# Kernel optimization log

Hardware: AMD Instinct MI355X
Metric: run time of the kernel (lower is better)

## Reference

```python
import jax, jax.numpy as jnp
import numpy as np

N_NODES = 50000
N_EDGES = 1600000
H1, F1 = 6, 16   # conv1 heads/filters
H2, F2 = 6, 24   # conv2 heads/filters
D_IN = 11
NEG_SLOPE = 0.2
EPS = 1e-12


def gat_layer(x, src, dst, W, a_src, a_dst, heads, filt):
    # x: [N, Din], W: [Din, heads*filt], a_src/a_dst: [heads, filt]
    N = x.shape[0]
    h = (x @ W).reshape(N, heads, filt)                      # [N,H,F]
    alpha_s = jnp.einsum('nhf,hf->nh', h, a_src)             # [N,H]
    alpha_d = jnp.einsum('nhf,hf->nh', h, a_dst)             # [N,H]
    e = jax.nn.leaky_relu(alpha_s[src] + alpha_d[dst], NEG_SLOPE)  # [E,H]
    # softmax over incoming edges of each dst node (segment softmax)
    m = jax.ops.segment_max(e, dst, num_segments=N)          # [N,H]
    m = jnp.where(jnp.isfinite(m), m, 0.0)
    ex = jnp.exp(e - m[dst])                                 # [E,H]
    denom = jax.ops.segment_sum(ex, dst, num_segments=N)     # [N,H]
    att = ex / (denom[dst] + EPS)                            # [E,H]
    msg = h[src] * att[:, :, None]                           # [E,H,F]
    out = jax.ops.segment_sum(msg, dst, num_segments=N)      # [N,H,F]
    return jax.nn.elu(out).reshape(N, heads * filt)


def setup_inputs() -> dict:
    key = jax.random.key(0)
    ks = jax.random.split(key, 12)
    x = jax.random.normal(ks[0], (N_NODES, D_IN), dtype=jnp.float32)
    src = jax.random.randint(ks[1], (N_EDGES,), 0, N_NODES, dtype=jnp.int32)
    dst = jax.random.randint(ks[2], (N_EDGES,), 0, N_NODES, dtype=jnp.int32)
    s = 0.1
    W1 = jax.random.normal(ks[3], (D_IN, H1 * F1), dtype=jnp.float32) * s
    a1s = jax.random.normal(ks[4], (H1, F1), dtype=jnp.float32) * s
    a1d = jax.random.normal(ks[5], (H1, F1), dtype=jnp.float32) * s
    W2 = jax.random.normal(ks[6], (H1 * F1, H2 * F2), dtype=jnp.float32) * s
    a2s = jax.random.normal(ks[7], (H2, F2), dtype=jnp.float32) * s
    a2d = jax.random.normal(ks[8], (H2, F2), dtype=jnp.float32) * s
    Wd = jax.random.normal(ks[9], (H2 * F2, 1), dtype=jnp.float32) * s
    bd = jnp.zeros((1,), dtype=jnp.float32)
    return {"x": x, "src": src, "dst": dst, "W1": W1, "a1s": a1s, "a1d": a1d,
            "W2": W2, "a2s": a2s, "a2d": a2d, "Wd": Wd, "bd": bd}


def reference(x, src, dst, W1, a1s, a1d, W2, a2s, a2d, Wd, bd):
    h = gat_layer(x, src, dst, W1, a1s, a1d, H1, F1)   # [N, 96]
    h = gat_layer(h, src, dst, W2, a2s, a2d, H2, F2)   # [N, 144]
    pooled = jnp.sum(h, axis=0).reshape(1, -1)         # [1, 144]
    norm = jnp.sqrt(jnp.sum(pooled * pooled, axis=1, keepdims=True))
    pooled = pooled / jnp.maximum(norm, 1e-12)         # F.normalize
    out = pooled @ Wd + bd                             # [1, 1], linear nonlin
    return jnp.squeeze(out, axis=1)                    # [1]
```

## Files before the change

### kernel.cpp

```cpp
#include <hip/hip_runtime.h>
#include <math.h>

#define NNODES 50000
#define NEDGES 1600000
#define NB 391
#define NBP 400

__device__ __forceinline__ float lrelu(float v) { return v > 0.f ? v : 0.2f * v; }

template<int SEL>
__device__ __forceinline__ float fp8d(unsigned u) {
    return __builtin_amdgcn_cvt_f32_fp8((int)u, SEL);
}

__global__ void padx_kernel(const float* __restrict__ x, float* __restrict__ xp, int N) {
    int t = blockIdx.x * blockDim.x + threadIdx.x;
    if (t >= N * 12) return;
    int n = t / 12, k = t - n * 12;
    xp[t] = (k < 11) ? x[n * 11 + k] : 0.f;
}

template<int DIN, int H, int F>
__global__ void va_kernel(const float* __restrict__ W, const float* __restrict__ a_s,
                          const float* __restrict__ a_d, float* __restrict__ va_s,
                          float* __restrict__ va_d, int DINEFF) {
    int t = threadIdx.x;
    if (t >= DIN * 8) return;
    int k = t / 8, h = t - k * 8;
    float s = 0.f, d = 0.f;
    if (h < H && k < DINEFF) {
        for (int f = 0; f < F; ++f) {
            float w = W[k * (H * F) + h * F + f];
            s = fmaf(w, a_s[h * F + f], s);
            d = fmaf(w, a_d[h * F + f], d);
        }
    }
    va_s[t] = s;
    va_d[t] = d;
}

template<int DIN>
__global__ void alphap_kernel(const float* __restrict__ X, const float* __restrict__ va_s,
                              const float* __restrict__ va_d, float* __restrict__ asp,
                              float* __restrict__ adp, int N) {
    __shared__ float vs[DIN * 8], vd[DIN * 8];
    for (int i = threadIdx.x; i < DIN * 8; i += blockDim.x) { vs[i] = va_s[i]; vd[i] = va_d[i]; }
    __syncthreads();
    int t = blockIdx.x * blockDim.x + threadIdx.x;
    if (t >= N * 8) return;
    int n = t / 8, h = t - n * 8;
    const float* xr = X + (size_t)n * DIN;
    float s = 0.f, d = 0.f;
    for (int k = 0; k < DIN; ++k) {
        float xv = xr[k];
        s = fmaf(xv, vs[k * 8 + h], s);
        d = fmaf(xv, vd[k * 8 + h], d);
    }
    asp[t] = s;
    adp[t] = d;
}

__global__ void bucket_hist_kernel(const int* __restrict__ dst, int* __restrict__ bcnt, int E) {
    __shared__ int h[NBP];
    for (int i = threadIdx.x; i < NBP; i += blockDim.x) h[i] = 0;
    __syncthreads();
    for (int e = blockIdx.x * blockDim.x + threadIdx.x; e < E; e += gridDim.x * blockDim.x)
        atomicAdd(&h[dst[e] >> 7], 1);
    __syncthreads();
    for (int i = threadIdx.x; i < NB; i += blockDim.x)
        if (h[i]) atomicAdd(&bcnt[i], h[i]);
}

__global__ void bucket_scan_kernel(const int* __restrict__ bcnt, int* __restrict__ bbase,
                                   int* __restrict__ bcur, int* __restrict__ off, int E) {
    __shared__ int ls[512];
    int t = threadIdx.x;
    int c = (t < NB) ? bcnt[t] : 0;
    ls[t] = c;
    __syncthreads();
    for (int o = 1; o < 512; o <<= 1) {
        int u = (t >= o) ? ls[t - o] : 0;
        __syncthreads();
        ls[t] += u;
        __syncthreads();
    }
    if (t < NB) {
        int ex = ls[t] - c;
        bbase[t] = ex;
        bcur[t] = ex;
    }
    if (t == 0) { bbase[NB] = E; off[NNODES] = E; }
}

#define BA_CHUNK 8192
#define BA_THREADS 1024
__global__ void binA_kernel(const int* __restrict__ src, const int* __restrict__ dst,
                            int* __restrict__ bcur, unsigned* __restrict__ tmp, int E) {
    __shared__ unsigned sv[BA_CHUNK];
    __shared__ unsigned short sb[BA_CHUNK];
    __shared__ int cnt[NBP], basel[NBP];
    int tid = threadIdx.x;
    for (int i = tid; i < NBP; i += BA_THREADS) cnt[i] = 0;
    __syncthreads();
    int e0 = blockIdx.x * BA_CHUNK;
    int lim = min(BA_CHUNK, E - e0);
#pragma unroll
    for (int k = 0; k < BA_CHUNK / BA_THREADS; ++k) {
        int i = k * BA_THREADS + tid;
        if (i < lim) {
            int s = src[e0 + i], d = dst[e0 + i];
            sv[i] = (unsigned)s | ((unsigned)(d & 127) << 17);
            int b = d >> 7;
            sb[i] = (unsigned short)b;
            atomicAdd(&cnt[b], 1);
        }
    }
    __syncthreads();
    for (int i = tid; i < NB; i += BA_THREADS)
        basel[i] = cnt[i] ? atomicAdd(&bcur[i], cnt[i]) : 0;
    __syncthreads();
#pragma unroll
    for (int k = 0; k < BA_CHUNK / BA_THREADS; ++k) {
        int i = k * BA_THREADS + tid;
        if (i < lim) {
            int pos = atomicAdd(&basel[sb[i]], 1);
            tmp[pos] = sv[i];
        }
    }
}

__global__ void binB_kernel(const int* __restrict__ bbase, const unsigned* __restrict__ tmp,
                            int* __restrict__ off, int* __restrict__ esrc, int N) {
    __shared__ int ncnt[128], ncur[128], ls[128];
    int b = blockIdx.x;
    int tid = threadIdx.x;
    int lo = bbase[b], hi = bbase[b + 1];
    if (tid < 128) ncnt[tid] = 0;
    __syncthreads();
    for (int i = lo + tid; i < hi; i += 256)
        atomicAdd(&ncnt[tmp[i] >> 17], 1);
    __syncthreads();
    if (tid < 128) ls[tid] = ncnt[tid];
    __syncthreads();
    for (int o = 1; o < 128; o <<= 1) {
        int u = (tid >= o && tid < 128) ? ls[tid - o] : 0;
        __syncthreads();
        if (tid < 128) ls[tid] += u;
        __syncthreads();
    }
    if (tid < 128) {
        int ex = lo + ls[tid] - ncnt[tid];
        int n = b * 128 + tid;
        if (n < N) off[n] = ex;
        ncur[tid] = ex;
    }
    __syncthreads();
    for (int i = lo + tid; i < hi; i += 256) {
        unsigned v = tmp[i];
        int pos = atomicAdd(&ncur[v >> 17], 1);
        esrc[pos] = (int)(v & 0x1FFFFu);
    }
}

#define G1_NODES 128
#define G1_THREADS (G1_NODES * 3)
#define G1_ECAP 4800
__global__ void gather1_kernel(const int* __restrict__ off, const int* __restrict__ esrc,
                               const float* __restrict__ asp, const float* __restrict__ adp,
                               const float* __restrict__ xp, float* __restrict__ aggX, int N) {
    __shared__ int se[G1_ECAP];
    int li = threadIdx.x;
    int n0 = blockIdx.x * G1_NODES;
    int nend = min(n0 + G1_NODES, N);
    int base = off[n0];
    int cnt = off[nend] - base;
    bool staged = (cnt <= G1_ECAP);
    if (staged) for (int i = li; i < cnt; i += G1_THREADS) se[i] = esrc[base + i];
    __syncthreads();
    int node = n0 + li / 3;
    int j = li % 3;
    if (node >= N) return;
    const float4 advA = *(const float4*)(adp + (size_t)node * 8);
    const float2 advB = *(const float2*)(adp + (size_t)node * 8 + 4);
    const float4* xp4 = (const float4*)xp;
    int p0 = off[node], p1 = off[node + 1];
    float4 ac[6];
    float d[6];
#pragma unroll
    for (int u = 0; u < 6; ++u) { ac[u] = make_float4(0.f, 0.f, 0.f, 0.f); d[u] = 0.f; }
#define G1_EDGE(asA, asB, xv)                                                        \
    {                                                                                \
        float a0 = __expf(lrelu(asA.x + advA.x));                                    \
        float a1 = __expf(lrelu(asA.y + advA.y));                                    \
        float a2 = __expf(lrelu(asA.z + advA.z));                                    \
        float a3 = __expf(lrelu(asA.w + advA.w));                                    \
        float a4 = __expf(lrelu(asB.x + advB.x));                                    \
        float a5 = __expf(lrelu(asB.y + advB.y));                                    \
        d[0] += a0; d[1] += a1; d[2] += a2; d[3] += a3; d[4] += a4; d[5] += a5;      \
        ac[0].x = fmaf(a0, xv.x, ac[0].x); ac[0].y = fmaf(a0, xv.y, ac[0].y);        \
        ac[0].z = fmaf(a0, xv.z, ac[0].z); ac[0].w = fmaf(a0, xv.w, ac[0].w);        \
        ac[1].x = fmaf(a1, xv.x, ac[1].x); ac[1].y = fmaf(a1, xv.y, ac[1].y);        \
        ac[1].z = fmaf(a1, xv.z, ac[1].z); ac[1].w = fmaf(a1, xv.w, ac[1].w);        \
        ac[2].x = fmaf(a2, xv.x, ac[2].x); ac[2].y = fmaf(a2, xv.y, ac[2].y);        \
        ac[2].z = fmaf(a2, xv.z, ac[2].z); ac[2].w = fmaf(a2, xv.w, ac[2].w);        \
        ac[3].x = fmaf(a3, xv.x, ac[3].x); ac[3].y = fmaf(a3, xv.y, ac[3].y);        \
        ac[3].z = fmaf(a3, xv.z, ac[3].z); ac[3].w = fmaf(a3, xv.w, ac[3].w);        \
        ac[4].x = fmaf(a4, xv.x, ac[4].x); ac[4].y = fmaf(a4, xv.y, ac[4].y);        \
        ac[4].z = fmaf(a4, xv.z, ac[4].z); ac[4].w = fmaf(a4, xv.w, ac[4].w);        \
        ac[5].x = fmaf(a5, xv.x, ac[5].x); ac[5].y = fmaf(a5, xv.y, ac[5].y);        \
        ac[5].z = fmaf(a5, xv.z, ac[5].z); ac[5].w = fmaf(a5, xv.w, ac[5].w);        \
    }
#define G1_LOOP(FS)                                                                  \
    {                                                                                \
        for (; q + 4 <= qe; q += 4) {                                                \
            int s0 = FS(q), s1 = FS(q + 1), s2 = FS(q + 2), s3 = FS(q + 3);          \
            float4 A0 = *(const float4*)(asp + (size_t)s0 * 8);                      \
            float2 B0 = *(const float2*)(asp + (size_t)s0 * 8 + 4);                  \
            float4 X0 = xp4[(size_t)s0 * 3 + j];                                     \
            float4 A1 = *(const float4*)(asp + (size_t)s1 * 8);                      \
            float2 B1 = *(const float2*)(asp + (size_t)s1 * 8 + 4);                  \
            float4 X1 = xp4[(size_t)s1 * 3 + j];                                     \
            float4 A2 = *(const float4*)(asp + (size_t)s2 * 8);                      \
            float2 B2 = *(const float2*)(asp + (size_t)s2 * 8 + 4);                  \
            float4 X2 = xp4[(size_t)s2 * 3 + j];                                     \
            float4 A3 = *(const float4*)(asp + (size_t)s3 * 8);                      \
            float2 B3 = *(const float2*)(asp + (size_t)s3 * 8 + 4);                  \
            float4 X3 = xp4[(size_t)s3 * 3 + j];                                     \
            G1_EDGE(A0, B0, X0) G1_EDGE(A1, B1, X1)                                  \
            G1_EDGE(A2, B2, X2) G1_EDGE(A3, B3, X3)                                  \
        }                                                                            \
        for (; q < qe; ++q) {                                                        \
            int s0 = FS(q);                                                          \
            float4 A0 = *(const float4*)(asp + (size_t)s0 * 8);                      \
            float2 B0 = *(const float2*)(asp + (size_t)s0 * 8 + 4);                  \
            float4 X0 = xp4[(size_t)s0 * 3 + j];                                     \
            G1_EDGE(A0, B0, X0)                                                      \
        }                                                                            \
    }
#define G1_SE(i) se[i]
#define G1_GE(i) esrc[i]
    if (staged) {
        int q = p0 - base, qe = p1 - base;
        G1_LOOP(G1_SE)
    } else {
        int q = p0, qe = p1;
        G1_LOOP(G1_GE)
    }
#undef G1_EDGE
#undef G1_LOOP
    float4* o4 = (float4*)aggX;
#pragma unroll
    for (int u = 0; u < 6; ++u) {
        float r = 1.f / (d[u] + 1e-12f);
        float4 a = ac[u];
        a.x *= r; a.y *= r; a.z *= r; a.w *= r;
        o4[((size_t)node * 6 + u) * 3 + j] = a;
    }
}

__global__ void gemmL1_kernel(const float* __restrict__ aggX, const float* __restrict__ W1,
                              float* __restrict__ out1, int N) {
    __shared__ float Wl[12 * 96];
    for (int i = threadIdx.x; i < 12 * 96; i += blockDim.x) Wl[i] = (i < 11 * 96) ? W1[i] : 0.f;
    __syncthreads();
    int t = blockIdx.x * blockDim.x + threadIdx.x;
    if (t >= N * 24) return;
    int n = t / 24, q = t - n * 24;
    int h = q / 4, c = q * 4;
    const float* ag = aggX + ((size_t)n * 6 + h) * 12;
    float4 acc = {0, 0, 0, 0};
#pragma unroll
    for (int k = 0; k < 12; ++k) {
        float xv = ag[k];
        acc.x = fmaf(xv, Wl[k * 96 + c + 0], acc.x);
        acc.y = fmaf(xv, Wl[k * 96 + c + 1], acc.y);
        acc.z = fmaf(xv, Wl[k * 96 + c + 2], acc.z);
        acc.w = fmaf(xv, Wl[k * 96 + c + 3], acc.w);
    }
    acc.x = acc.x > 0.f ? acc.x : expm1f(acc.x);
    acc.y = acc.y > 0.f ? acc.y : expm1f(acc.y);
    acc.z = acc.z > 0.f ? acc.z : expm1f(acc.z);
    acc.w = acc.w > 0.f ? acc.w : expm1f(acc.w);
    ((float4*)out1)[(size_t)n * 24 + q] = acc;
}

template<int DIN, int C, int NPT>
__global__ void gemm_fp8_kernel(const float* __restrict__ X, const float* __restrict__ W,
                                unsigned* __restrict__ Out, int N) {
    constexpr int Q = C / 4;
    __shared__ float4 Wl[DIN * Q];
    for (int i = threadIdx.x; i < DIN * Q; i += blockDim.x) Wl[i] = ((const float4*)W)[i];
    __syncthreads();
    int t = blockIdx.x * blockDim.x + threadIdx.x;
    int g = t / Q, q = t - g * Q;
    int n0 = g * NPT;
    if (n0 >= N) return;
    const float4* X4 = (const float4*)X;
    float4 acc[NPT];
#pragma unroll
    for (int u = 0; u < NPT; ++u) acc[u] = make_float4(0.f, 0.f, 0.f, 0.f);
#pragma unroll 2
    for (int k4 = 0; k4 < DIN / 4; ++k4) {
        float4 xv[NPT];
#pragma unroll
        for (int u = 0; u < NPT; ++u) xv[u] = X4[(size_t)(n0 + u) * (DIN / 4) + k4];
#pragma unroll
        for (int i = 0; i < 4; ++i) {
            float4 w = Wl[(k4 * 4 + i) * Q + q];
#pragma unroll
            for (int u = 0; u < NPT; ++u) {
                float xs = (i == 0) ? xv[u].x : (i == 1) ? xv[u].y : (i == 2) ? xv[u].z : xv[u].w;
                acc[u].x = fmaf(xs, w.x, acc[u].x);
                acc[u].y = fmaf(xs, w.y, acc[u].y);
                acc[u].z = fmaf(xs, w.z, acc[u].z);
                acc[u].w = fmaf(xs, w.w, acc[u].w);
            }
        }
    }
#pragma unroll
    for (int u = 0; u < NPT; ++u) {
        int pk = __builtin_amdgcn_cvt_pk_fp8_f32(acc[u].x, acc[u].y, 0, false);
        pk     = __builtin_amdgcn_cvt_pk_fp8_f32(acc[u].z, acc[u].w, pk, true);
        Out[(size_t)(n0 + u) * Q + q] = (unsigned)pk;
    }
}

#define G2_NODES 32
#define G2_TPN 18
#define G2_THREADS (G2_NODES * G2_TPN)
#define G2_ECAP 1600
__global__ void gather2_kernel(const int* __restrict__ off, const int* __restrict__ esrc,
                               const float* __restrict__ asp, const float* __restrict__ adp,
                               const uint2* __restrict__ h2t2, float* __restrict__ pooled, int N) {
    __shared__ float sp[144];
    __shared__ int se[G2_ECAP];
    int li = threadIdx.x;
    int n0 = blockIdx.x * G2_NODES;
    int nend = min(n0 + G2_NODES, N);
    int base = off[n0];
    int cnt = off[nend] - base;
    bool staged = (cnt <= G2_ECAP);
    if (staged) for (int i = li; i < cnt; i += G2_THREADS) se[i] = esrc[base + i];
    if (li < 144) sp[li] = 0.f;
    __syncthreads();
    int node = n0 + li / G2_TPN;
    int j = li % G2_TPN;
    if (node < N) {
        int h = j / 3;
        float adv = adp[(size_t)node * 8 + h];
        int p0 = off[node], p1 = off[node + 1];
        float acc[8];
#pragma unroll
        for (int c = 0; c < 8; ++c) acc[c] = 0.f;
        float den = 0.f;
#define G2_EDGE(ev, v)                                                     \
    {                                                                      \
        float att = __expf(lrelu(ev + adv));                               \
        den += att;                                                        \
        acc[0] = fmaf(att, fp8d<0>(v.x), acc[0]);                          \
        acc[1] = fmaf(att, fp8d<1>(v.x), acc[1]);                          \
        acc[2] = fmaf(att, fp8d<2>(v.x), acc[2]);                          \
        acc[3] = fmaf(att, fp8d<3>(v.x), acc[3]);                          \
        acc[4] = fmaf(att, fp8d<0>(v.y), acc[4]);                          \
        acc[5] = fmaf(att, fp8d<1>(v.y), acc[5]);                          \
        acc[6] = fmaf(att, fp8d<2>(v.y), acc[6]);                          \
        acc[7] = fmaf(att, fp8d<3>(v.y), acc[7]);                          \
    }
#define G2_LOOP(FS)                                                                        \
    {                                                                                      \
        for (; q + 4 <= qe; q += 4) {                                                      \
            int s0 = FS(q), s1 = FS(q + 1), s2 = FS(q + 2), s3 = FS(q + 3);                \
            float e0 = asp[(size_t)s0 * 8 + h], e1 = asp[(size_t)s1 * 8 + h];              \
            float e2 = asp[(size_t)s2 * 8 + h], e3 = asp[(size_t)s3 * 8 + h];              \
            uint2 v0 = h2t2[(size_t)s0 * 18 + j], v1 = h2t2[(size_t)s1 * 18 + j];          \
            uint2 v2 = h2t2[(size_t)s2 * 18 + j], v3 = h2t2[(size_t)s3 * 18 + j];          \
            G2_EDGE(e0, v0) G2_EDGE(e1, v1) G2_EDGE(e2, v2) G2_EDGE(e3, v3)                \
        }                                                                                  \
        for (; q < qe; ++q) {                                                              \
            int s0 = FS(q);                                                                \
            float e0 = asp[(size_t)s0 * 8 + h];                                            \
            uint2 v0 = h2t2[(size_t)s0 * 18 + j];                                          \
            G2_EDGE(e0, v0)                                                                \
        }                                                                                  \
    }
#define G2_SE(i) se[i]
#define G2_GE(i) esrc[i]
        if (staged) {
            int q = p0 - base, qe = p1 - base;
            G2_LOOP(G2_SE)
        } else {
            int q = p0, qe = p1;
            G2_LOOP(G2_GE)
        }
#undef G2_EDGE
#undef G2_LOOP
        float rd = 1.f / (den + 1e-12f);
        int cb = 8 * j;
#pragma unroll
        for (int c = 0; c < 8; ++c) {
            float vv = acc[c] * rd;
            vv = vv > 0.f ? vv : expm1f(vv);
            atomicAdd(&sp[cb + c], vv);
        }
    }
    __syncthreads();
    if (li < 144) atomicAdd(&pooled[li], sp[li]);
}

__global__ void final_kernel(const float* __restrict__ pooled, const float* __restrict__ Wd,
                             const float* __restrict__ bd, float* __restrict__ out) {
    int l = threadIdx.x;
    float ss = 0.f, dot = 0.f;
    for (int c = l; c < 144; c += 64) {
        float p = pooled[c];
        ss = fmaf(p, p, ss);
        dot = fmaf(p, Wd[c], dot);
    }
#pragma unroll
    for (int o = 32; o > 0; o >>= 1) {
        ss += __shfl_down(ss, o);
        dot += __shfl_down(dot, o);
    }
    if (l == 0) out[0] = dot / fmaxf(sqrtf(ss), 1e-12f) + bd[0];
}

extern "C" void kernel_launch(void* const* d_in, const int* in_sizes, int n_in,
                              void* d_out, int out_size, void* d_ws, size_t ws_size,
                              hipStream_t stream) {
    const float* x   = (const float*)d_in[0];
    const int*   src = (const int*)  d_in[1];
    const int*   dst = (const int*)  d_in[2];
    const float* W1  = (const float*)d_in[3];
    const float* a1s = (const float*)d_in[4];
    const float* a1d = (const float*)d_in[5];
    const float* W2  = (const float*)d_in[6];
    const float* a2s = (const float*)d_in[7];
    const float* a2d = (const float*)d_in[8];
    const float* Wd  = (const float*)d_in[9];
    const float* bd  = (const float*)d_in[10];

    const int N = NNODES, E = NEDGES;
    float* ws = (float*)d_ws;
    float* xp    = ws;
    float* asp1  = xp + (size_t)N * 12;
    float* adp1  = asp1 + (size_t)N * 8;
    float* aggX  = adp1 + (size_t)N * 8;
    float* out1  = aggX + (size_t)N * 72;
    unsigned* h2t = (unsigned*)(out1 + (size_t)N * 96);
    float* asp2  = out1 + (size_t)N * 96 + (size_t)N * 72;
    float* adp2  = asp2 + (size_t)N * 8;
    float* va1s  = adp2 + (size_t)N * 8;
    float* va1d  = va1s + 96;
    float* va2s  = va1d + 96;
    float* va2d  = va2s + 768;
    float* pooled = va2d + 768;
    int*   off   = (int*)(pooled + 144);
    int*   esrc  = off + (N + 1);
    unsigned* tmp = (unsigned*)(esrc + E);
    int*   bcnt  = (int*)(tmp + E);
    int*   bbase = bcnt + NB;
    int*   bcur  = bbase + (NB + 1);

    const int B = 256;
    auto grid = [](long total, int b) { return (int)((total + b - 1) / b); };

    hipMemsetAsync(bcnt, 0, NB * sizeof(int), stream);
    bucket_hist_kernel<<<256, 256, 0, stream>>>(dst, bcnt, E);
    bucket_scan_kernel<<<1, 512, 0, stream>>>(bcnt, bbase, bcur, off, E);
    binA_kernel<<<grid(E, BA_CHUNK), BA_THREADS, 0, stream>>>(src, dst, bcur, tmp, E);
    binB_kernel<<<NB, 256, 0, stream>>>(bbase, tmp, off, esrc, N);

    padx_kernel<<<grid((long)N * 12, B), B, 0, stream>>>(x, xp, N);
    va_kernel<12, 6, 16><<<1, 96, 0, stream>>>(W1, a1s, a1d, va1s, va1d, 11);
    alphap_kernel<12><<<grid((long)N * 8, B), B, 0, stream>>>(xp, va1s, va1d, asp1, adp1, N);
    gather1_kernel<<<grid(N, G1_NODES), G1_THREADS, 0, stream>>>(off, esrc, asp1, adp1, xp, aggX, N);
    gemmL1_kernel<<<grid((long)N * 24, B), B, 0, stream>>>(aggX, W1, out1, N);

    va_kernel<96, 6, 24><<<1, 768, 0, stream>>>(W2, a2s, a2d, va2s, va2d, 96);
    alphap_kernel<96><<<grid((long)N * 8, B), B, 0, stream>>>(out1, va2s, va2d, asp2, adp2, N);
    gemm_fp8_kernel<96, 144, 2><<<grid((long)(N / 2) * 36, 1024), 1024, 0, stream>>>(out1, W2, h2t, N);
    hipMemsetAsync(pooled, 0, 144 * sizeof(float), stream);
    gather2_kernel<<<grid(N, G2_NODES), G2_THREADS, 0, stream>>>(off, esrc, asp2, adp2,
                                                                 (const uint2*)h2t, pooled, N);

    final_kernel<<<1, 64, 0, stream>>>(pooled, Wd, bd, (float*)d_out);
}
```

Measured before the change: 232.8 us.

## Merge setup kernels and memsets into one prep launch; resize gather2 blocks

Padding x, both attention-vector precomputations and the zeroing of the bucket counters and pooled buffer are folded into one multi-role prep kernel. This removes four launches and two memset calls from the stream. Separately, gather2 now uses 28 nodes per block in 512-thread blocks, with the extra lanes idle, instead of 32 nodes in 576 threads. That raises the block count and wastes a few lanes but gives power-of-two block sizes. The prep launch now runs before binning, so the va computations are no longer placed next to the layers that use them.

Result: faster. 215.5 us (-7.4%).

```diff
diff --git a/kernel.cpp b/kernel.cpp
--- a/kernel.cpp
+++ b/kernel.cpp
@@ -13,30 +13,53 @@
     return __builtin_amdgcn_cvt_f32_fp8((int)u, SEL);
 }
 
-__global__ void padx_kernel(const float* __restrict__ x, float* __restrict__ xp, int N) {
-    int t = blockIdx.x * blockDim.x + threadIdx.x;
-    if (t >= N * 12) return;
-    int n = t / 12, k = t - n * 12;
-    xp[t] = (k < 11) ? x[n * 11 + k] : 0.f;
-}
-
-template<int DIN, int H, int F>
-__global__ void va_kernel(const float* __restrict__ W, const float* __restrict__ a_s,
-                          const float* __restrict__ a_d, float* __restrict__ va_s,
-                          float* __restrict__ va_d, int DINEFF) {
-    int t = threadIdx.x;
-    if (t >= DIN * 8) return;
-    int k = t / 8, h = t - k * 8;
-    float s = 0.f, d = 0.f;
-    if (h < H && k < DINEFF) {
-        for (int f = 0; f < F; ++f) {
-            float w = W[k * (H * F) + h * F + f];
-            s = fmaf(w, a_s[h * F + f], s);
-            d = fmaf(w, a_d[h * F + f], d);
-        }
-    }
-    va_s[t] = s;
-    va_d[t] = d;
+__global__ void prep_kernel(const float* __restrict__ x, float* __restrict__ xp,
+                            const float* __restrict__ W1, const float* __restrict__ a1s,
+                            const float* __restrict__ a1d, float* __restrict__ va1s,
+                            float* __restrict__ va1d,
+                            const float* __restrict__ W2, const float* __restrict__ a2s,
+                            const float* __restrict__ a2d, float* __restrict__ va2s,
+                            float* __restrict__ va2d,
+                            int* __restrict__ bcnt, float* __restrict__ pooled, int N) {
+    int b = blockIdx.x, t = threadIdx.x;
+    if (b == 0) {
+        if (t < 96) {
+            int k = t >> 3, h = t & 7;
+            float s = 0.f, d = 0.f;
+            if (h < 6 && k < 11) {
+                for (int f = 0; f < 16; ++f) {
+                    float w = W1[k * 96 + h * 16 + f];
+                    s = fmaf(w, a1s[h * 16 + f], s);
+                    d = fmaf(w, a1d[h * 16 + f], d);
+                }
+            }
+            va1s[t] = s;
+            va1d[t] = d;
+        }
+    } else if (b == 1) {
+        if (t < 768) {
+            int k = t >> 3, h = t & 7;
+            float s = 0.f, d = 0.f;
+            if (h < 6) {
+                for (int f = 0; f < 24; ++f) {
+                    float w = W2[k * 144 + h * 24 + f];
+                    s = fmaf(w, a2s[h * 24 + f], s);
+                    d = fmaf(w, a2d[h * 24 + f], d);
+                }
+            }
+            va2s[t] = s;
+            va2d[t] = d;
+        }
+    } else if (b == 2) {
+        if (t < NB) bcnt[t] = 0;
+        if (t >= 512 && t < 512 + 144) pooled[t - 512] = 0.f;
+    } else {
+        int i = (b - 3) * 768 + t;
+        if (i < N * 12) {
+            int n = i / 12, k = i - n * 12;
+            xp[i] = (k < 11) ? x[n * 11 + k] : 0.f;
+        }
+    }
 }
 
 template<int DIN>
@@ -325,9 +348,10 @@
     }
 }
 
-#define G2_NODES 32
+#define G2_NODES 28
 #define G2_TPN 18
-#define G2_THREADS (G2_NODES * G2_TPN)
+#define G2_THREADS 512
+#define G2_ACTIVE (G2_NODES * G2_TPN)
 #define G2_ECAP 1600
 __global__ void gather2_kernel(const int* __restrict__ off, const int* __restrict__ esrc,
                                const float* __restrict__ asp, const float* __restrict__ adp,
@@ -345,7 +369,7 @@
     __syncthreads();
     int node = n0 + li / G2_TPN;
     int j = li % G2_TPN;
-    if (node < N) {
+    if (li < G2_ACTIVE && node < N) {
         int h = j / 3;
         float adv = adp[(size_t)node * 8 + h];
         int p0 = off[node], p1 = off[node + 1];
@@ -464,22 +488,20 @@
     const int B = 256;
     auto grid = [](long total, int b) { return (int)((total + b - 1) / b); };
 
-    hipMemsetAsync(bcnt, 0, NB * sizeof(int), stream);
+    prep_kernel<<<3 + grid((long)N * 12, 768), 768, 0, stream>>>(
+        x, xp, W1, a1s, a1d, va1s, va1d, W2, a2s, a2d, va2s, va2d, bcnt, pooled, N);
+
     bucket_hist_kernel<<<256, 256, 0, stream>>>(dst, bcnt, E);
     bucket_scan_kernel<<<1, 512, 0, stream>>>(bcnt, bbase, bcur, off, E);
     binA_kernel<<<grid(E, BA_CHUNK), BA_THREADS, 0, stream>>>(src, dst, bcur, tmp, E);
     binB_kernel<<<NB, 256, 0, stream>>>(bbase, tmp, off, esrc, N);
 
-    padx_kernel<<<grid((long)N * 12, B), B, 0, stream>>>(x, xp, N);
-    va_kernel<12, 6, 16><<<1, 96, 0, stream>>>(W1, a1s, a1d, va1s, va1d, 11);
     alphap_kernel<12><<<grid((long)N * 8, B), B, 0, stream>>>(xp, va1s, va1d, asp1, adp1, N);
     gather1_kernel<<<grid(N, G1_NODES), G1_THREADS, 0, stream>>>(off, esrc, asp1, adp1, xp, aggX, N);
     gemmL1_kernel<<<grid((long)N * 24, B), B, 0, stream>>>(aggX, W1, out1, N);
 
-    va_kernel<96, 6, 24><<<1, 768, 0, stream>>>(W2, a2s, a2d, va2s, va2d, 96);
     alphap_kernel<96><<<grid((long)N * 8, B), B, 0, stream>>>(out1, va2s, va2d, asp2, adp2, N);
     gemm_fp8_kernel<96, 144, 2><<<grid((long)(N / 2) * 36, 1024), 1024, 0, stream>>>(out1, W2, h2t, N);
-    hipMemsetAsync(pooled, 0, 144 * sizeof(float), stream);
     gather2_kernel<<<grid(N, G2_NODES), G2_THREADS, 0, stream>>>(off, esrc, asp2, adp2,
                                                                  (const uint2*)h2t, pooled, N);
 
```
